# Performance work log

Hardware: AMD Instinct MI355X
Metric: run time of the kernel (lower is better)

The kernel has to match this reference:

```python
import jax, jax.numpy as jnp
import numpy as np
from jax import lax

N, CIN, P, CH, COUT = 1024, 3, 14, 256, 3
DN = ('NCHW', 'OIHW', 'NCHW')


def _conv(x, w, b, pad=1):
    y = lax.conv_general_dilated(x, w, (1, 1), [(pad, pad), (pad, pad)], dimension_numbers=DN)
    return y + b[None, :, None, None]


def _conv_transpose(x, w_t, b):
    # PyTorch ConvTranspose2d(k=3, stride=2, padding=1, output_padding=1):
    # equivalent to conv with lhs_dilation=2, padding (k-1-p, k-1-p+op) = (1, 2),
    # kernel with in/out swapped and spatially flipped. w_t: [in, out, 3, 3]
    w = jnp.flip(jnp.transpose(w_t, (1, 0, 2, 3)), axis=(2, 3))  # [out, in, 3, 3]
    y = lax.conv_general_dilated(x, w, (1, 1), [(1, 2), (1, 2)], lhs_dilation=(2, 2),
                                 dimension_numbers=DN)
    return y + b[None, :, None, None]


def setup_inputs() -> dict:
    key = jax.random.key(0)
    ks = jax.random.split(key, 16)
    s3 = lambda cin: 1.0 / np.sqrt(cin * 9)
    inp = {"x": jax.random.normal(ks[0], (N, CIN, P, P), dtype=jnp.float32)}
    inp["w1"] = jax.random.normal(ks[1], (CH, CIN, 3, 3), jnp.float32) * s3(CIN)
    inp["b1"] = jnp.zeros((CH,), jnp.float32)
    inp["w2"] = jax.random.normal(ks[2], (CH, CH, 3, 3), jnp.float32) * s3(CH)
    inp["b2"] = jnp.zeros((CH,), jnp.float32)
    inp["w3"] = jax.random.normal(ks[3], (CH, CH, 3, 3), jnp.float32) * s3(CH)
    inp["b3"] = jnp.zeros((CH,), jnp.float32)
    inp["w4"] = jax.random.normal(ks[4], (CH, CH, 3, 3), jnp.float32) * s3(CH)
    inp["b4"] = jnp.zeros((CH,), jnp.float32)
    inp["wt"] = jax.random.normal(ks[5], (CH, CH, 3, 3), jnp.float32) * s3(CH)  # [in, out, kh, kw]
    inp["bt"] = jnp.zeros((CH,), jnp.float32)
    inp["w5"] = jax.random.normal(ks[6], (COUT, CH, 1, 1), jnp.float32) * (1.0 / np.sqrt(CH))
    inp["b5"] = jnp.zeros((COUT,), jnp.float32)
    return inp


def reference(x, w1, b1, w2, b2, w3, b3, w4, b4, wt, bt, w5, b5):
    h = jax.nn.relu(_conv(x, w1, b1))
    h = jax.nn.relu(_conv(h, w2, b2))
    h = jax.nn.relu(_conv(h, w3, b3))
    h = jax.nn.relu(_conv(h, w4, b4))
    h = jax.nn.relu(_conv_transpose(h, wt, bt))  # [N, 256, 2P, 2P]
    h = _conv(h, w5, b5, pad=0)                   # 1x1 conv -> [N, 3, 2P, 2P]
    return jax.nn.sigmoid(h)
```

## Files before the change

### kernel.cpp

```cpp
#include <hip/hip_runtime.h>
#include <hip/hip_fp16.h>

typedef _Float16 half8 __attribute__((ext_vector_type(8)));
typedef _Float16 half4 __attribute__((ext_vector_type(4)));
typedef float floatx4 __attribute__((ext_vector_type(4)));

#define PLANE 65536
#define PK_ELEMS 589824

__global__ void repack_kernel(const float* __restrict__ w2, const float* __restrict__ w3,
                              const float* __restrict__ w4, const float* __restrict__ wt,
                              _Float16* __restrict__ pk) {
    int t = blockIdx.x * 256 + threadIdx.x;
    int l = t & 63;
    int idx = t >> 6;
    int nt = idx & 15; idx >>= 4;
    int ks = idx & 7;  idx >>= 3;
    int tap = idx % 9;
    int layer = idx / 9;
    int co = nt * 16 + (l & 15);
    int ci0 = ks * 32 + (l >> 4) * 8;
    const float* w = (layer == 0) ? w2 : (layer == 1) ? w3 : (layer == 2) ? w4 : wt;
    _Float16* dst = pk + (size_t)layer * PK_ELEMS + (((size_t)(tap * 8 + ks) * 16 + nt) * 64 + l) * 8;
    if (layer < 3) {
        for (int j = 0; j < 8; ++j)
            dst[j] = (_Float16)w[(co * 256 + (ci0 + j)) * 9 + tap];
    } else {
        int ky = tap / 3, kx = tap % 3;
        for (int j = 0; j < 8; ++j)
            dst[j] = (_Float16)w[((ci0 + j) * 256 + co) * 9 + (2 - ky) * 3 + (2 - kx)];
    }
}

__global__ __launch_bounds__(1024, 4) void conv1_kernel(const float* __restrict__ x,
                                                        const float* __restrict__ w1,
                                                        const float* __restrict__ b1,
                                                        _Float16* __restrict__ act) {
    __shared__ float inl[3][16][16];
    __shared__ float lw[256 * 27];
    __shared__ float lb1[256];
    int n = blockIdx.x, tid = threadIdx.x;
    if (tid < 768) ((float*)inl)[tid] = 0.f;
    __syncthreads();
    for (int i = tid; i < 3 * 196; i += 1024) {
        int ci = i / 196, r = i % 196, y = r / 14, xx = r % 14;
        inl[ci][y + 1][xx + 1] = x[(size_t)n * 588 + i];
    }
    for (int i = tid; i < 256 * 27; i += 1024) lw[i] = w1[i];
    if (tid < 256) lb1[tid] = b1[tid];
    __syncthreads();
    int p = tid >> 2, q = tid & 3;
    int py = p >> 4, px = p & 15;
    _Float16* ga = act + (size_t)n * PLANE + p * 256;
    int sw = (p & 7) << 3;
    if (py == 0 || py == 15 || px == 0 || px == 15) {
        for (int ci = 0; ci < 64; ++ci) { int co = q + ci * 4; ga[co ^ sw] = (_Float16)0.f; }
    } else {
        float vin[27];
        #pragma unroll
        for (int ci = 0; ci < 3; ++ci)
            #pragma unroll
            for (int ky = 0; ky < 3; ++ky)
                #pragma unroll
                for (int kx = 0; kx < 3; ++kx)
                    vin[ci * 9 + ky * 3 + kx] = inl[ci][py - 1 + ky][px - 1 + kx];
        for (int ci = 0; ci < 64; ++ci) {
            int co = q + ci * 4;
            float acc = lb1[co];
            const float* wp = &lw[co * 27];
            #pragma unroll
            for (int k = 0; k < 27; ++k) acc += vin[k] * wp[k];
            ga[co ^ sw] = (_Float16)fmaxf(acc, 0.f);
        }
    }
}


#define INIT_ACC(BIASPTR)                                                        \
    {                                                                            \
        _Pragma("unroll")                                                        \
        for (int ni = 0; ni < 4; ++ni) {                                         \
            floatx4 bv;                                                          \
            _Pragma("unroll")                                                    \
            for (int reg = 0; reg < 4; ++reg)                                    \
                bv[reg] = (BIASPTR)[(cg * 4 + ni) * 16 + kg * 4 + reg];          \
            _Pragma("unroll")                                                    \
            for (int i = 0; i < 7; ++i) acc[i][ni] = bv;                         \
        }                                                                        \
    }

#define ACCUM_TAP(PKT, DOFF)                                                     \
    {                                                                            \
        const _Float16* pkt_ = (PKT);                                            \
        _Pragma("unroll")                                                        \
        for (int ks = 0; ks < 8; ++ks) {                                         \
            half8 a0 = *(const half8*)(pkt_ + (((ks * 16) + cg * 4 + 0) * 64 + lane) * 8); \
            half8 a1 = *(const half8*)(pkt_ + (((ks * 16) + cg * 4 + 1) * 64 + lane) * 8); \
            half8 a2 = *(const half8*)(pkt_ + (((ks * 16) + cg * 4 + 2) * 64 + lane) * 8); \
            half8 a3 = *(const half8*)(pkt_ + (((ks * 16) + cg * 4 + 3) * 64 + lane) * 8); \
            _Pragma("unroll")                                                    \
            for (int j = 0; j < 7; ++j) {                                        \
                int ipx = pp[j] + (DOFF);                                        \
                int chunk = (ks * 4 + kg) ^ (ipx & 7);                           \
                half8 bb = *(const half8*)(plane + ipx * 256 + chunk * 8);       \
                acc[j][0] = __builtin_amdgcn_mfma_f32_16x16x32_f16(a0, bb, acc[j][0], 0, 0, 0); \
                acc[j][1] = __builtin_amdgcn_mfma_f32_16x16x32_f16(a1, bb, acc[j][1], 0, 0, 0); \
                acc[j][2] = __builtin_amdgcn_mfma_f32_16x16x32_f16(a2, bb, acc[j][2], 0, 0, 0); \
                acc[j][3] = __builtin_amdgcn_mfma_f32_16x16x32_f16(a3, bb, acc[j][3], 0, 0, 0); \
            }                                                                    \
        }                                                                        \
    }

#define EPILOGUE(RY, RX)                                                         \
    {                                                                            \
        _Pragma("unroll")                                                        \
        for (int i = 0; i < 7; ++i) {                                            \
            float s0 = 0.f, s1 = 0.f, s2 = 0.f;                                  \
            _Pragma("unroll")                                                    \
            for (int ni = 0; ni < 4; ++ni) {                                     \
                int co0 = (cg * 4 + ni) * 16 + kg * 4;                           \
                _Pragma("unroll")                                                \
                for (int reg = 0; reg < 4; ++reg) {                              \
                    float v = fmaxf(acc[i][ni][reg], 0.f);                       \
                    s0 += v * w5l[co0 + reg];                                    \
                    s1 += v * w5l[256 + co0 + reg];                              \
                    s2 += v * w5l[512 + co0 + reg];                              \
                }                                                                \
            }                                                                    \
            s0 += __shfl_xor(s0, 16, 64); s0 += __shfl_xor(s0, 32, 64);          \
            s1 += __shfl_xor(s1, 16, 64); s1 += __shfl_xor(s1, 32, 64);          \
            s2 += __shfl_xor(s2, 16, 64); s2 += __shfl_xor(s2, 32, 64);          \
            if (lane < 14) {                                                     \
                int pt_ = pg + 2 * i;                                            \
                int pix = (2 * pt_ + (RY)) * 28 + 2 * lane + (RX);               \
                atomicAdd(&o3[pix * 3 + 0], s0);                                 \
                atomicAdd(&o3[pix * 3 + 1], s1);                                 \
                atomicAdd(&o3[pix * 3 + 2], s2);                                 \
            }                                                                    \
        }                                                                        \
    }

__global__ __launch_bounds__(512, 2) void fused_kernel(const _Float16* __restrict__ act,
                                                       const _Float16* __restrict__ pk,
                                                       const float* __restrict__ b2,
                                                       const float* __restrict__ b3,
                                                       const float* __restrict__ b4,
                                                       const float* __restrict__ bt,
                                                       const float* __restrict__ w5,
                                                       const float* __restrict__ b5,
                                                       float* __restrict__ out) {
    __shared__ _Float16 plane[PLANE];
    __shared__ float o3[2352];
    __shared__ float w5l[768];
    int n = blockIdx.x, tid = threadIdx.x;
    const _Float16* ga = act + (size_t)n * PLANE;
    #pragma unroll
    for (int i = 0; i < 16; ++i)
        *(uint4*)(plane + (i * 512 + tid) * 8) = *(const uint4*)(ga + (i * 512 + tid) * 8);
    for (int i = tid; i < 2352; i += 512) o3[i] = b5[i % 3];
    for (int i = tid; i < 768; i += 512) w5l[i] = w5[i];

    int lane = tid & 63, wid = tid >> 6;
    int cg = wid >> 1, pg = wid & 1;
    int col = lane & 15, kg = lane >> 4;

    int pp[7];
    {
        int xc = (col < 14) ? col : 13;
        #pragma unroll
        for (int i = 0; i < 7; ++i) pp[i] = (pg + 2 * i + 1) * 16 + xc + 1;
    }
    bool colok = (col < 14);
    __syncthreads();

    floatx4 acc[7][4];

    for (int L = 0; L < 3; ++L) {
        const _Float16* pkL = pk + (size_t)L * PK_ELEMS;
        const float* bias = (L == 0) ? b2 : (L == 1) ? b3 : b4;
        INIT_ACC(bias)
        for (int tap = 0; tap < 9; ++tap) {
            int doff = (tap / 3) * 16 + (tap % 3) - 17;
            ACCUM_TAP(pkL + (size_t)tap * 65536, doff)
        }
        __syncthreads();
        #pragma unroll
        for (int i = 0; i < 7; ++i) {
            int ppix = pp[i];
            int sw = (ppix & 7) << 3;
            if (colok) {
                #pragma unroll
                for (int ni = 0; ni < 4; ++ni) {
                    int co0 = (cg * 4 + ni) * 16 + kg * 4;
                    half4 h;
                    #pragma unroll
                    for (int reg = 0; reg < 4; ++reg) h[reg] = (_Float16)fmaxf(acc[i][ni][reg], 0.f);
                    *(half4*)(plane + ppix * 256 + (co0 ^ sw)) = h;
                }
            }
        }
        __syncthreads();
    }

    const _Float16* pkT = pk + (size_t)3 * PK_ELEMS;
    INIT_ACC(bt)
    ACCUM_TAP(pkT + 4 * 65536, 0)
    EPILOGUE(0, 0)
    INIT_ACC(bt)
    ACCUM_TAP(pkT + 3 * 65536, 0)
    ACCUM_TAP(pkT + 5 * 65536, 1)
    EPILOGUE(0, 1)
    INIT_ACC(bt)
    ACCUM_TAP(pkT + 1 * 65536, 0)
    ACCUM_TAP(pkT + 7 * 65536, 16)
    EPILOGUE(1, 0)
    INIT_ACC(bt)
    ACCUM_TAP(pkT + 0 * 65536, 0)
    ACCUM_TAP(pkT + 2 * 65536, 1)
    ACCUM_TAP(pkT + 6 * 65536, 16)
    ACCUM_TAP(pkT + 8 * 65536, 17)
    EPILOGUE(1, 1)

    __syncthreads();
    size_t ob = (size_t)n * 2352;
    for (int i = tid; i < 2352; i += 512) {
        int pix = i / 3, c = i % 3;
        float v = o3[i];
        out[ob + (size_t)c * 784 + pix] = 1.f / (1.f + __expf(-v));
    }
}

extern "C" void kernel_launch(void* const* d_in, const int* in_sizes, int n_in,
                              void* d_out, int out_size, void* d_ws, size_t ws_size,
                              hipStream_t stream) {
    const float* x  = (const float*)d_in[0];
    const float* w1 = (const float*)d_in[1];
    const float* b1 = (const float*)d_in[2];
    const float* w2 = (const float*)d_in[3];
    const float* b2 = (const float*)d_in[4];
    const float* w3 = (const float*)d_in[5];
    const float* b3 = (const float*)d_in[6];
    const float* w4 = (const float*)d_in[7];
    const float* b4 = (const float*)d_in[8];
    const float* wt = (const float*)d_in[9];
    const float* bt = (const float*)d_in[10];
    const float* w5 = (const float*)d_in[11];
    const float* b5 = (const float*)d_in[12];

    size_t need = ((size_t)1024 * PLANE + 4 * (size_t)PK_ELEMS) * sizeof(_Float16);
    if (ws_size < need) return;

    _Float16* act = (_Float16*)d_ws;
    _Float16* pk  = act + (size_t)1024 * PLANE;

    repack_kernel<<<1152, 256, 0, stream>>>(w2, w3, w4, wt, pk);
    conv1_kernel<<<1024, 1024, 0, stream>>>(x, w1, b1, act);
    fused_kernel<<<1024, 512, 0, stream>>>(act, pk, b2, b3, b4, bt, w5, b5, (float*)d_out);
}
```

Before: 1.013 ms.

## Reuse loaded activation rows across all taps with DPP lane shifts

Reorders the conv loops so that each K-slice loads 15 activation rows from shared memory into registers once and reuses them for all nine taps. Horizontal tap offsets are produced by DPP row shifts across lanes instead of extra LDS reads, and column mapping shifts to lanes 1..14. It also raises wave priority around MFMA bursts and makes the wave id uniform via readfirstlane. The aim is to cut LDS read traffic, at the cost of much higher register pressure from 15 half8 buffers plus the accumulators, which risks spills at 512 threads with 2 blocks per CU.

```diff
diff --git a/kernel.cpp b/kernel.cpp
--- a/kernel.cpp
+++ b/kernel.cpp
@@ -4,9 +4,19 @@
 typedef _Float16 half8 __attribute__((ext_vector_type(8)));
 typedef _Float16 half4 __attribute__((ext_vector_type(4)));
 typedef float floatx4 __attribute__((ext_vector_type(4)));
+typedef int intx4 __attribute__((ext_vector_type(4)));
 
 #define PLANE 65536
 #define PK_ELEMS 589824
+
+template <int CTRL>
+__device__ __forceinline__ half8 dpp_shift(half8 v) {
+    intx4 s = __builtin_bit_cast(intx4, v), r;
+    #pragma unroll
+    for (int d = 0; d < 4; ++d)
+        r[d] = __builtin_amdgcn_update_dpp(0, s[d], CTRL, 0xf, 0xf, false);
+    return __builtin_bit_cast(half8, r);
+}
 
 __global__ void repack_kernel(const float* __restrict__ w2, const float* __restrict__ w3,
                               const float* __restrict__ w4, const float* __restrict__ wt,
@@ -89,26 +99,25 @@
         }                                                                        \
     }
 
-#define ACCUM_TAP(PKT, DOFF)                                                     \
+#define TAPB(PKL, TAP, DY, DX)                                                   \
     {                                                                            \
-        const _Float16* pkt_ = (PKT);                                            \
+        const _Float16* pa_ = (PKL) + (TAP) * 65536 + (ks * 16 + cg * 4) * 512 + lane * 8; \
+        half8 a0_ = *(const half8*)(pa_);                                        \
+        half8 a1_ = *(const half8*)(pa_ + 512);                                  \
+        half8 a2_ = *(const half8*)(pa_ + 1024);                                 \
+        half8 a3_ = *(const half8*)(pa_ + 1536);                                 \
+        __builtin_amdgcn_s_setprio(1);                                           \
         _Pragma("unroll")                                                        \
-        for (int ks = 0; ks < 8; ++ks) {                                         \
-            half8 a0 = *(const half8*)(pkt_ + (((ks * 16) + cg * 4 + 0) * 64 + lane) * 8); \
-            half8 a1 = *(const half8*)(pkt_ + (((ks * 16) + cg * 4 + 1) * 64 + lane) * 8); \
-            half8 a2 = *(const half8*)(pkt_ + (((ks * 16) + cg * 4 + 2) * 64 + lane) * 8); \
-            half8 a3 = *(const half8*)(pkt_ + (((ks * 16) + cg * 4 + 3) * 64 + lane) * 8); \
-            _Pragma("unroll")                                                    \
-            for (int j = 0; j < 7; ++j) {                                        \
-                int ipx = pp[j] + (DOFF);                                        \
-                int chunk = (ks * 4 + kg) ^ (ipx & 7);                           \
-                half8 bb = *(const half8*)(plane + ipx * 256 + chunk * 8);       \
-                acc[j][0] = __builtin_amdgcn_mfma_f32_16x16x32_f16(a0, bb, acc[j][0], 0, 0, 0); \
-                acc[j][1] = __builtin_amdgcn_mfma_f32_16x16x32_f16(a1, bb, acc[j][1], 0, 0, 0); \
-                acc[j][2] = __builtin_amdgcn_mfma_f32_16x16x32_f16(a2, bb, acc[j][2], 0, 0, 0); \
-                acc[j][3] = __builtin_amdgcn_mfma_f32_16x16x32_f16(a3, bb, acc[j][3], 0, 0, 0); \
-            }                                                                    \
+        for (int i = 0; i < 7; ++i) {                                            \
+            half8 bb = (DX) == 0 ? B_[2 * i + 1 + (DY)]                          \
+                     : ((DX) < 0 ? dpp_shift<0x111>(B_[2 * i + 1 + (DY)])        \
+                                 : dpp_shift<0x101>(B_[2 * i + 1 + (DY)]));      \
+            acc[i][0] = __builtin_amdgcn_mfma_f32_16x16x32_f16(a0_, bb, acc[i][0], 0, 0, 0); \
+            acc[i][1] = __builtin_amdgcn_mfma_f32_16x16x32_f16(a1_, bb, acc[i][1], 0, 0, 0); \
+            acc[i][2] = __builtin_amdgcn_mfma_f32_16x16x32_f16(a2_, bb, acc[i][2], 0, 0, 0); \
+            acc[i][3] = __builtin_amdgcn_mfma_f32_16x16x32_f16(a3_, bb, acc[i][3], 0, 0, 0); \
         }                                                                        \
+        __builtin_amdgcn_s_setprio(0);                                           \
     }
 
 #define EPILOGUE(RY, RX)                                                         \
@@ -130,9 +139,8 @@
             s0 += __shfl_xor(s0, 16, 64); s0 += __shfl_xor(s0, 32, 64);          \
             s1 += __shfl_xor(s1, 16, 64); s1 += __shfl_xor(s1, 32, 64);          \
             s2 += __shfl_xor(s2, 16, 64); s2 += __shfl_xor(s2, 32, 64);          \
-            if (lane < 14) {                                                     \
-                int pt_ = pg + 2 * i;                                            \
-                int pix = (2 * pt_ + (RY)) * 28 + 2 * lane + (RX);               \
+            if (lane >= 1 && lane <= 14) {                                       \
+                int pix = (2 * (pg + 2 * i) + (RY)) * 28 + 2 * (lane - 1) + (RX); \
                 atomicAdd(&o3[pix * 3 + 0], s0);                                 \
                 atomicAdd(&o3[pix * 3 + 1], s1);                                 \
                 atomicAdd(&o3[pix * 3 + 2], s2);                                 \
@@ -160,17 +168,14 @@
     for (int i = tid; i < 2352; i += 512) o3[i] = b5[i % 3];
     for (int i = tid; i < 768; i += 512) w5l[i] = w5[i];
 
-    int lane = tid & 63, wid = tid >> 6;
+    int lane = tid & 63;
+    int wid = __builtin_amdgcn_readfirstlane(tid >> 6);
     int cg = wid >> 1, pg = wid & 1;
     int col = lane & 15, kg = lane >> 4;
-
-    int pp[7];
-    {
-        int xc = (col < 14) ? col : 13;
-        #pragma unroll
-        for (int i = 0; i < 7; ++i) pp[i] = (pg + 2 * i + 1) * 16 + xc + 1;
-    }
-    bool colok = (col < 14);
+    int sw = (col & 7) << 3;
+    bool colok = (col >= 1 && col <= 14);
+    const _Float16* pb = plane + pg * 4096 + col * 256;
+
     __syncthreads();
 
     floatx4 acc[7][4];
@@ -179,23 +184,31 @@
         const _Float16* pkL = pk + (size_t)L * PK_ELEMS;
         const float* bias = (L == 0) ? b2 : (L == 1) ? b3 : b4;
         INIT_ACC(bias)
-        for (int tap = 0; tap < 9; ++tap) {
-            int doff = (tap / 3) * 16 + (tap % 3) - 17;
-            ACCUM_TAP(pkL + (size_t)tap * 65536, doff)
+        #pragma clang loop unroll(disable)
+        for (int ks = 0; ks < 8; ++ks) {
+            int kk = ((ks * 4 + kg) << 3) ^ sw;
+            half8 B_[15];
+            #pragma unroll
+            for (int j = 0; j < 15; ++j)
+                B_[j] = *(const half8*)(pb + j * 4096 + kk);
+            #pragma unroll
+            for (int tap = 0; tap < 9; ++tap) {
+                const int dy = tap / 3 - 1, dx = tap % 3 - 1;
+                TAPB(pkL, tap, dy, dx)
+            }
         }
         __syncthreads();
         #pragma unroll
         for (int i = 0; i < 7; ++i) {
-            int ppix = pp[i];
-            int sw = (ppix & 7) << 3;
             if (colok) {
+                int p = (pg + 2 * i + 1) * 16 + col;
                 #pragma unroll
                 for (int ni = 0; ni < 4; ++ni) {
                     int co0 = (cg * 4 + ni) * 16 + kg * 4;
                     half4 h;
                     #pragma unroll
                     for (int reg = 0; reg < 4; ++reg) h[reg] = (_Float16)fmaxf(acc[i][ni][reg], 0.f);
-                    *(half4*)(plane + ppix * 256 + (co0 ^ sw)) = h;
+                    *(half4*)(plane + p * 256 + (co0 ^ sw)) = h;
                 }
             }
         }
@@ -204,21 +217,49 @@
 
     const _Float16* pkT = pk + (size_t)3 * PK_ELEMS;
     INIT_ACC(bt)
-    ACCUM_TAP(pkT + 4 * 65536, 0)
+    #pragma clang loop unroll(disable)
+    for (int ks = 0; ks < 8; ++ks) {
+        int kk = ((ks * 4 + kg) << 3) ^ sw;
+        half8 B_[15];
+        #pragma unroll
+        for (int j = 1; j < 15; ++j) B_[j] = *(const half8*)(pb + j * 4096 + kk);
+        TAPB(pkT, 4, 0, 0)
+    }
     EPILOGUE(0, 0)
     INIT_ACC(bt)
-    ACCUM_TAP(pkT + 3 * 65536, 0)
-    ACCUM_TAP(pkT + 5 * 65536, 1)
+    #pragma clang loop unroll(disable)
+    for (int ks = 0; ks < 8; ++ks) {
+        int kk = ((ks * 4 + kg) << 3) ^ sw;
+        half8 B_[15];
+        #pragma unroll
+        for (int j = 1; j < 15; ++j) B_[j] = *(const half8*)(pb + j * 4096 + kk);
+        TAPB(pkT, 3, 0, 0)
+        TAPB(pkT, 5, 0, 1)
+    }
     EPILOGUE(0, 1)
     INIT_ACC(bt)
-    ACCUM_TAP(pkT + 1 * 65536, 0)
-    ACCUM_TAP(pkT + 7 * 65536, 16)
+    #pragma clang loop unroll(disable)
+    for (int ks = 0; ks < 8; ++ks) {
+        int kk = ((ks * 4 + kg) << 3) ^ sw;
+        half8 B_[15];
+        #pragma unroll
+        for (int j = 1; j < 15; ++j) B_[j] = *(const half8*)(pb + j * 4096 + kk);
+        TAPB(pkT, 1, 0, 0)
+        TAPB(pkT, 7, 1, 0)
+    }
     EPILOGUE(1, 0)
     INIT_ACC(bt)
-    ACCUM_TAP(pkT + 0 * 65536, 0)
-    ACCUM_TAP(pkT + 2 * 65536, 1)
-    ACCUM_TAP(pkT + 6 * 65536, 16)
-    ACCUM_TAP(pkT + 8 * 65536, 17)
+    #pragma clang loop unroll(disable)
+    for (int ks = 0; ks < 8; ++ks) {
+        int kk = ((ks * 4 + kg) << 3) ^ sw;
+        half8 B_[15];
+        #pragma unroll
+        for (int j = 1; j < 15; ++j) B_[j] = *(const half8*)(pb + j * 4096 + kk);
+        TAPB(pkT, 0, 0, 0)
+        TAPB(pkT, 2, 0, 1)
+        TAPB(pkT, 6, 1, 0)
+        TAPB(pkT, 8, 1, 1)
+    }
     EPILOGUE(1, 1)
 
     __syncthreads();
```

Result: faster. 918.6 us (-9.3%).
